# Kernel tuning notes

Measured on AMD Instinct MI355X. Metric: run time of the kernel, lower is better.

## Reference

```python
import jax, jax.numpy as jnp
import numpy as np

B, H, S, D = 1, 16, 8192, 64
WINDOW = 1024  # window_size from init; also used as the query block size


def setup_inputs() -> dict:
    key = jax.random.key(0)
    kq, kk, kv = jax.random.split(key, 3)
    Q = jax.random.normal(kq, (B, H, S, D), dtype=jnp.float32)
    K = jax.random.normal(kk, (B, H, S, D), dtype=jnp.float32)
    V = jax.random.normal(kv, (B, H, S, D), dtype=jnp.float32)
    return {"Q": Q, "K": K, "V": V}


def _sliding_window_attn(Q, K, V, window):
    # Banded causal attention: query q attends kv with 0 <= q - kv <= window.
    # Tile queries into blocks of size W=window; each query block i only needs
    # kv positions [i*W - W, i*W + W), i.e. a 2W-wide local slice. This honors
    # the block-sparse structure instead of materializing an SxS score matrix.
    b, h, s, d = Q.shape
    W = window
    nb = s // W  # number of query blocks
    # Pad K,V by W zeros at the front so every block slice is in-bounds.
    Kp = jnp.pad(K, ((0, 0), (0, 0), (W, 0), (0, 0)))
    Vp = jnp.pad(V, ((0, 0), (0, 0), (W, 0), (0, 0)))
    # Local kv indices for each block: block i covers padded positions [i*W, i*W+2W).
    idx = jnp.arange(nb)[:, None] * W + jnp.arange(2 * W)[None, :]  # [nb, 2W]
    Kb = Kp[:, :, idx, :]  # [B,H,nb,2W,D]
    Vb = Vp[:, :, idx, :]  # [B,H,nb,2W,D]
    Qb = Q.reshape(b, h, nb, W, d)  # [B,H,nb,W,D]

    scale = np.float32(1.0 / np.sqrt(d))  # flex_attention default scaling
    scores = jnp.einsum('bhnqd,bhnkd->bhnqk', Qb, Kb) * scale  # [B,H,nb,W,2W]

    # Global positions: q_global = i*W + qi ; kv_global = i*W + kj - W.
    # Mask conds: q>=kv  <=> qi >= kj - W ;  q-kv<=W  <=> qi <= kj ; kv_global>=0.
    qi = jnp.arange(W)[:, None]          # [W,1]
    kj = jnp.arange(2 * W)[None, :]      # [1,2W]
    rel_mask = (qi <= kj) & (qi >= kj - W)                        # [W,2W]
    kv_global = jnp.arange(nb)[:, None, None] * W + kj[None] - W  # [nb,1,2W]
    mask = rel_mask[None] & (kv_global >= 0)                      # [nb,W,2W]

    neg = jnp.finfo(scores.dtype).min
    scores = jnp.where(mask[None, None], scores, neg)
    attn = jax.nn.softmax(scores, axis=-1)
    out = jnp.einsum('bhnqk,bhnkd->bhnqd', attn, Vb)
    return out.reshape(b, h, s, d)


def reference(Q, K, V):
    return _sliding_window_attn(Q, K, V, WINDOW)
```

## Files before the change

kernel.cpp:

```cpp
#include <hip/hip_runtime.h>
#include <stdint.h>

namespace {
constexpr int kH = 16;
constexpr int kS = 8192;
constexpr int kD = 64;
constexpr int kW = 1024;

typedef __attribute__((ext_vector_type(4)))  float float4_t;
typedef __attribute__((ext_vector_type(16))) float f32x16;
typedef __attribute__((ext_vector_type(8)))  short bf16x8;
typedef __attribute__((ext_vector_type(8)))  short short8_t;

__device__ __forceinline__ unsigned short f2bf(float f) {
    union { float fv; uint32_t u; } c; c.fv = f;
    return (unsigned short)((c.u + 0x7fffu + ((c.u >> 16) & 1u)) >> 16);
}

__device__ __forceinline__ float fexp2(float x) {
#if __has_builtin(__builtin_amdgcn_exp2f)
    return __builtin_amdgcn_exp2f(x);
#else
    return exp2f(x);
#endif
}

__device__ __forceinline__ void gload16(const void* g, char* l) {
    __builtin_amdgcn_global_load_lds(
        (const __attribute__((address_space(1))) void*)g,
        (__attribute__((address_space(3))) void*)l, 16, 0, 0);
}

__global__ __launch_bounds__(256)
void prep_k(const float* __restrict__ K, unsigned short* __restrict__ Kb) {
    const int i = (blockIdx.x * 256 + threadIdx.x) * 8;
    float4_t a = *(const float4_t*)(K + i);
    float4_t b = *(const float4_t*)(K + i + 4);
    short8_t o;
    #pragma unroll
    for (int j = 0; j < 4; ++j) { o[j] = (short)f2bf(a[j]); o[j + 4] = (short)f2bf(b[j]); }
    *(short8_t*)(Kb + i) = o;
}

__global__ __launch_bounds__(256)
void prep_v(const float* __restrict__ V, unsigned short* __restrict__ Vt) {
    __shared__ float tile[64][65];
    const int h = blockIdx.y;
    const int s0 = blockIdx.x * 64;
    const int tid = threadIdx.x;
    const size_t hb = (size_t)h * kS * kD;
    #pragma unroll
    for (int it = 0; it < 4; ++it) {
        const int n = tid + it * 256;
        const int s = n >> 4, d0 = (n & 15) * 4;
        float4_t v = *(const float4_t*)(V + hb + (size_t)(s0 + s) * kD + d0);
        tile[s][d0 + 0] = v[0]; tile[s][d0 + 1] = v[1];
        tile[s][d0 + 2] = v[2]; tile[s][d0 + 3] = v[3];
    }
    __syncthreads();
    #pragma unroll
    for (int it = 0; it < 2; ++it) {
        const int n = tid + it * 256;
        const int d = n >> 3, sc = (n & 7) * 8;
        short8_t o;
        #pragma unroll
        for (int j = 0; j < 8; ++j) o[j] = (short)f2bf(tile[sc + j][d]);
        *(short8_t*)(Vt + (size_t)h * kD * kS + (size_t)d * kS + s0 + sc) = o;
    }
}

__global__ __launch_bounds__(256, 4)
void swa_main(const float* __restrict__ Qg, const unsigned short* __restrict__ Kb,
              const unsigned short* __restrict__ Vt, float* __restrict__ Og) {
    __shared__ __align__(16) char lds[2][16384];

    const int lid  = blockIdx.x;
    const int swz  = (lid & 7) * 128 + (lid >> 3);
    const int h    = swz >> 6;
    const int qblk = swz & 63;

    const int tid  = threadIdx.x;
    const int wv   = tid >> 6;
    const int lane = tid & 63;
    const int lq   = lane & 31;
    const int hi   = lane >> 5;

    const int q0b = qblk * 128;
    const int qs  = q0b + wv * 32;
    const int q   = qs + lq;
    const size_t hb  = (size_t)h * kS * kD;
    const size_t hbv = (size_t)h * kD * kS;

    constexpr float qscale = 0.125f * 1.44269504f;
    bf16x8 qf[4];
    {
        const float* qp = Qg + hb + (size_t)q * kD + hi * 8;
        #pragma unroll
        for (int c = 0; c < 4; ++c) {
            float4_t a = *(const float4_t*)(qp + c * 16);
            float4_t b = *(const float4_t*)(qp + c * 16 + 4);
            bf16x8 f;
            #pragma unroll
            for (int j = 0; j < 4; ++j) {
                f[j]     = (short)f2bf(a[j] * qscale);
                f[j + 4] = (short)f2bf(b[j] * qscale);
            }
            qf[c] = f;
        }
    }

    f32x16 acc[2];
    #pragma unroll
    for (int hf = 0; hf < 2; ++hf)
        #pragma unroll
        for (int r = 0; r < 16; ++r) acc[hf][r] = 0.f;
    float l4[4] = {0.f, 0.f, 0.f, 0.f};

    const int kstart = (q0b >= kW) ? q0b - kW : 0;
    const int nt     = (q0b + 128 - kstart) >> 6;

    int srcK[2], srcV[2];
    #pragma unroll
    for (int i = 0; i < 2; ++i) {
        const int n = tid + i * 256;
        const int c = n ^ ((n >> 3) & 7);
        srcK[i] = (c >> 3) * 64 + (c & 7) * 8;
        srcV[i] = (c >> 3) * kS + (c & 7) * 8;
    }
    const unsigned short* KbH = Kb + hb;
    const unsigned short* VtH = Vt + hbv;

    auto stage = [&](int buf, int kb) {
        const unsigned short* Kt = KbH + (size_t)kb * 64;
        const unsigned short* Vq = VtH + kb;
        #pragma unroll
        for (int i = 0; i < 2; ++i) {
            const int db = i * 4096 + wv * 1024;
            gload16(Kt + srcK[i], &lds[buf][db]);
            gload16(Vq + srcV[i], &lds[buf][8192 + db]);
        }
    };

    stage(0, kstart);
    for (int t = 0; t < nt; ++t) {
        const int kb  = kstart + t * 64;
        const int kbn = (t + 1 < nt) ? kb + 64 : kb;
        stage((t + 1) & 1, kbn);
        asm volatile("s_waitcnt vmcnt(4)" ::: "memory");
        __builtin_amdgcn_s_barrier();
        asm volatile("" ::: "memory");

        const char* Kl = lds[t & 1];
        const char* Vl = lds[t & 1] + 8192;

        #pragma unroll
        for (int half = 0; half < 2; ++half) {
            const int kh = kb + half * 32;
            if (kh <= qs && kh >= qs - kW) {
                const int krow = half * 32 + lq;
                const int ksw  = (krow & 7) << 4;
                bf16x8 kf[4];
                #pragma unroll
                for (int c = 0; c < 4; ++c)
                    kf[c] = *(const bf16x8*)(Kl + ((krow * 128 + c * 32 + hi * 16) ^ ksw));

                f32x16 st;
                #pragma unroll
                for (int r = 0; r < 16; ++r) st[r] = 0.f;
                __builtin_amdgcn_s_setprio(1);
                #pragma unroll
                for (int c = 0; c < 4; ++c)
                    st = __builtin_amdgcn_mfma_f32_32x32x16_bf16(kf[c], qf[c], st, 0, 0, 0);
                __builtin_amdgcn_s_setprio(0);

                const int vsw = (lq & 7) << 4;
                bf16x8 vf[4];
                #pragma unroll
                for (int dh = 0; dh < 2; ++dh)
                    #pragma unroll
                    for (int kc = 0; kc < 2; ++kc)
                        vf[dh * 2 + kc] = *(const bf16x8*)(
                            Vl + (((dh * 32 + lq) * 128 + half * 64 + kc * 32 + hi * 16) ^ vsw));

                float p[16];
                const bool interior = (kh <= qs - 32) && (kh >= qs - 992);
                if (interior) {
                    #pragma unroll
                    for (int r = 0; r < 16; ++r) p[r] = fexp2(st[r]);
                } else {
                    #pragma unroll
                    for (int r = 0; r < 16; ++r) {
                        const int ki = kh + (r & 3) + 8 * (r >> 2) + 4 * hi;
                        const bool ok = (ki <= q) && (ki + kW >= q);
                        const float e = fexp2(st[r]);
                        p[r] = ok ? e : 0.f;
                    }
                }
                #pragma unroll
                for (int r = 0; r < 16; ++r) l4[r & 3] += p[r];

                unsigned int wrd[8];
                #pragma unroll
                for (int j = 0; j < 8; ++j)
                    asm("v_cvt_pk_bf16_f32 %0, %1, %2" : "=v"(wrd[j]) : "v"(p[2 * j]), "v"(p[2 * j + 1]));
                asm("v_permlane32_swap_b32 %0, %1" : "+v"(wrd[0]), "+v"(wrd[2]));
                asm("v_permlane32_swap_b32 %0, %1" : "+v"(wrd[1]), "+v"(wrd[3]));
                asm("v_permlane32_swap_b32 %0, %1" : "+v"(wrd[4]), "+v"(wrd[6]));
                asm("v_permlane32_swap_b32 %0, %1" : "+v"(wrd[5]), "+v"(wrd[7]));
                union U { unsigned int u[4]; bf16x8 v; };
                U u0, u1;
                u0.u[0] = wrd[0]; u0.u[1] = wrd[1]; u0.u[2] = wrd[2]; u0.u[3] = wrd[3];
                u1.u[0] = wrd[4]; u1.u[1] = wrd[5]; u1.u[2] = wrd[6]; u1.u[3] = wrd[7];

                __builtin_amdgcn_s_setprio(1);
                acc[0] = __builtin_amdgcn_mfma_f32_32x32x16_bf16(vf[0], u0.v, acc[0], 0, 0, 0);
                acc[1] = __builtin_amdgcn_mfma_f32_32x32x16_bf16(vf[2], u0.v, acc[1], 0, 0, 0);
                acc[0] = __builtin_amdgcn_mfma_f32_32x32x16_bf16(vf[1], u1.v, acc[0], 0, 0, 0);
                acc[1] = __builtin_amdgcn_mfma_f32_32x32x16_bf16(vf[3], u1.v, acc[1], 0, 0, 0);
                __builtin_amdgcn_s_setprio(0);
            }
        }

        asm volatile("" ::: "memory");
        __builtin_amdgcn_s_barrier();
        asm volatile("" ::: "memory");
    }

    float l = (l4[0] + l4[1]) + (l4[2] + l4[3]);
    l += __shfl_xor(l, 32);
    const float rl = 1.f / l;
    float* op = Og + hb + (size_t)q * kD;
    #pragma unroll
    for (int g = 0; g < 4; ++g) {
        float4_t o0, o1;
        #pragma unroll
        for (int j = 0; j < 4; ++j) {
            o0[j] = acc[0][g * 4 + j] * rl;
            o1[j] = acc[1][g * 4 + j] * rl;
        }
        *(float4_t*)(op + g * 8 + hi * 4)      = o0;
        *(float4_t*)(op + 32 + g * 8 + hi * 4) = o1;
    }
}
}

extern "C" void kernel_launch(void* const* d_in, const int* in_sizes, int n_in,
                              void* d_out, int out_size, void* d_ws, size_t ws_size,
                              hipStream_t stream) {
    (void)in_sizes; (void)n_in; (void)out_size; (void)ws_size;
    const float* Q = (const float*)d_in[0];
    const float* K = (const float*)d_in[1];
    const float* V = (const float*)d_in[2];
    float* O = (float*)d_out;
    unsigned short* Kb = (unsigned short*)d_ws;
    unsigned short* Vt = Kb + (size_t)kH * kS * kD;

    prep_k<<<dim3(kH * kS * kD / 2048), dim3(256), 0, stream>>>(K, Kb);
    prep_v<<<dim3(kS / 64, kH), dim3(256), 0, stream>>>(V, Vt);
    swa_main<<<dim3(1024), dim3(256), 0, stream>>>(Q, Kb, Vt, O);
}
```

Baseline: 71.86 us.

## Fuse K bf16 conversion into attention kernel, dropping separate prep_k pass

```diff
diff --git a/kernel.cpp b/kernel.cpp
--- a/kernel.cpp
+++ b/kernel.cpp
@@ -11,6 +11,7 @@
 typedef __attribute__((ext_vector_type(16))) float f32x16;
 typedef __attribute__((ext_vector_type(8)))  short bf16x8;
 typedef __attribute__((ext_vector_type(8)))  short short8_t;
+typedef __attribute__((ext_vector_type(4)))  unsigned int u32x4;
 
 __device__ __forceinline__ unsigned short f2bf(float f) {
     union { float fv; uint32_t u; } c; c.fv = f;
@@ -31,21 +32,24 @@
         (__attribute__((address_space(3))) void*)l, 16, 0, 0);
 }
 
-__global__ __launch_bounds__(256)
-void prep_k(const float* __restrict__ K, unsigned short* __restrict__ Kb) {
-    const int i = (blockIdx.x * 256 + threadIdx.x) * 8;
-    float4_t a = *(const float4_t*)(K + i);
-    float4_t b = *(const float4_t*)(K + i + 4);
-    short8_t o;
-    #pragma unroll
-    for (int j = 0; j < 4; ++j) { o[j] = (short)f2bf(a[j]); o[j + 4] = (short)f2bf(b[j]); }
-    *(short8_t*)(Kb + i) = o;
-}
+#define P_TO_FRAGS(P, U0, U1)                                                            \
+    {                                                                                    \
+        unsigned int wrd[8];                                                             \
+        _Pragma("unroll")                                                                \
+        for (int j = 0; j < 8; ++j)                                                      \
+            asm("v_cvt_pk_bf16_f32 %0, %1, %2" : "=v"(wrd[j]) : "v"(P[2*j]), "v"(P[2*j+1])); \
+        asm("v_permlane32_swap_b32 %0, %1" : "+v"(wrd[0]), "+v"(wrd[2]));                \
+        asm("v_permlane32_swap_b32 %0, %1" : "+v"(wrd[1]), "+v"(wrd[3]));                \
+        asm("v_permlane32_swap_b32 %0, %1" : "+v"(wrd[4]), "+v"(wrd[6]));                \
+        asm("v_permlane32_swap_b32 %0, %1" : "+v"(wrd[5]), "+v"(wrd[7]));                \
+        U0.u[0] = wrd[0]; U0.u[1] = wrd[1]; U0.u[2] = wrd[2]; U0.u[3] = wrd[3];          \
+        U1.u[0] = wrd[4]; U1.u[1] = wrd[5]; U1.u[2] = wrd[6]; U1.u[3] = wrd[7];          \
+    }
 
 __global__ __launch_bounds__(256)
 void prep_v(const float* __restrict__ V, unsigned short* __restrict__ Vt) {
     __shared__ float tile[64][65];
-    const int h = blockIdx.y;
+    const int h  = blockIdx.y;
     const int s0 = blockIdx.x * 64;
     const int tid = threadIdx.x;
     const size_t hb = (size_t)h * kS * kD;
@@ -65,12 +69,12 @@
         short8_t o;
         #pragma unroll
         for (int j = 0; j < 8; ++j) o[j] = (short)f2bf(tile[sc + j][d]);
-        *(short8_t*)(Vt + (size_t)h * kD * kS + (size_t)d * kS + s0 + sc) = o;
+        *(short8_t*)(Vt + hb + (size_t)d * kS + s0 + sc) = o;
     }
 }
 
 __global__ __launch_bounds__(256, 4)
-void swa_main(const float* __restrict__ Qg, const unsigned short* __restrict__ Kb,
+void swa_main(const float* __restrict__ Qg, const float* __restrict__ Kg,
               const unsigned short* __restrict__ Vt, float* __restrict__ Og) {
     __shared__ __align__(16) char lds[2][16384];
 
@@ -88,8 +92,7 @@
     const int q0b = qblk * 128;
     const int qs  = q0b + wv * 32;
     const int q   = qs + lq;
-    const size_t hb  = (size_t)h * kS * kD;
-    const size_t hbv = (size_t)h * kD * kS;
+    const size_t hb = (size_t)h * kS * kD;
 
     constexpr float qscale = 0.125f * 1.44269504f;
     bf16x8 qf[4];
@@ -111,54 +114,89 @@
 
     f32x16 acc[2];
     #pragma unroll
-    for (int hf = 0; hf < 2; ++hf)
-        #pragma unroll
-        for (int r = 0; r < 16; ++r) acc[hf][r] = 0.f;
+    for (int r = 0; r < 16; ++r) { acc[0][r] = 0.f; acc[1][r] = 0.f; }
     float l4[4] = {0.f, 0.f, 0.f, 0.f};
 
     const int kstart = (q0b >= kW) ? q0b - kW : 0;
     const int nt     = (q0b + 128 - kstart) >> 6;
 
-    int srcK[2], srcV[2];
+    const int r0 = tid >> 3, g8 = (tid & 7) * 8;
+    const int r1 = r0 + 32;
+    const int kdst0 = (r0 * 128 + g8 * 2) ^ ((r0 & 7) << 4);
+    const int kdst1 = (r1 * 128 + g8 * 2) ^ ((r1 & 7) << 4);
+    const float* KgH = Kg + hb;
+
+    int srcV[2];
     #pragma unroll
     for (int i = 0; i < 2; ++i) {
         const int n = tid + i * 256;
         const int c = n ^ ((n >> 3) & 7);
-        srcK[i] = (c >> 3) * 64 + (c & 7) * 8;
         srcV[i] = (c >> 3) * kS + (c & 7) * 8;
     }
-    const unsigned short* KbH = Kb + hb;
-    const unsigned short* VtH = Vt + hbv;
-
-    auto stage = [&](int buf, int kb) {
-        const unsigned short* Kt = KbH + (size_t)kb * 64;
-        const unsigned short* Vq = VtH + kb;
-        #pragma unroll
-        for (int i = 0; i < 2; ++i) {
-            const int db = i * 4096 + wv * 1024;
-            gload16(Kt + srcK[i], &lds[buf][db]);
-            gload16(Vq + srcV[i], &lds[buf][8192 + db]);
-        }
-    };
-
-    stage(0, kstart);
+    const unsigned short* VtH = Vt + hb;
+
+    float4_t k0lo, k0hi, k1lo, k1hi;
+
+    union U { unsigned int u[4]; bf16x8 v; };
+
+#define LOAD_K(KB)                                                         \
+    {                                                                      \
+        const float* p0_ = KgH + (size_t)((KB) + r0) * kD + g8;            \
+        const float* p1_ = KgH + (size_t)((KB) + r1) * kD + g8;            \
+        k0lo = *(const float4_t*)(p0_);                                    \
+        k0hi = *(const float4_t*)(p0_ + 4);                                \
+        k1lo = *(const float4_t*)(p1_);                                    \
+        k1hi = *(const float4_t*)(p1_ + 4);                                \
+    }
+
+#define STAGE_V(BUF, KB)                                                   \
+    {                                                                      \
+        const unsigned short* vq_ = VtH + (KB);                            \
+        gload16(vq_ + srcV[0], &lds[BUF][8192 + wv * 1024]);               \
+        gload16(vq_ + srcV[1], &lds[BUF][8192 + 4096 + wv * 1024]);        \
+    }
+
+#define CVT_WRITE_K(BUF)                                                   \
+    {                                                                      \
+        unsigned int w0_, w1_, w2_, w3_;                                   \
+        u32x4 wv0_, wv1_;                                                  \
+        asm("v_cvt_pk_bf16_f32 %0, %1, %2" : "=v"(w0_) : "v"(k0lo[0]), "v"(k0lo[1])); \
+        asm("v_cvt_pk_bf16_f32 %0, %1, %2" : "=v"(w1_) : "v"(k0lo[2]), "v"(k0lo[3])); \
+        asm("v_cvt_pk_bf16_f32 %0, %1, %2" : "=v"(w2_) : "v"(k0hi[0]), "v"(k0hi[1])); \
+        asm("v_cvt_pk_bf16_f32 %0, %1, %2" : "=v"(w3_) : "v"(k0hi[2]), "v"(k0hi[3])); \
+        wv0_[0] = w0_; wv0_[1] = w1_; wv0_[2] = w2_; wv0_[3] = w3_;        \
+        asm("v_cvt_pk_bf16_f32 %0, %1, %2" : "=v"(w0_) : "v"(k1lo[0]), "v"(k1lo[1])); \
+        asm("v_cvt_pk_bf16_f32 %0, %1, %2" : "=v"(w1_) : "v"(k1lo[2]), "v"(k1lo[3])); \
+        asm("v_cvt_pk_bf16_f32 %0, %1, %2" : "=v"(w2_) : "v"(k1hi[0]), "v"(k1hi[1])); \
+        asm("v_cvt_pk_bf16_f32 %0, %1, %2" : "=v"(w3_) : "v"(k1hi[2]), "v"(k1hi[3])); \
+        wv1_[0] = w0_; wv1_[1] = w1_; wv1_[2] = w2_; wv1_[3] = w3_;        \
+        *(u32x4*)(&lds[BUF][kdst0]) = wv0_;                                \
+        *(u32x4*)(&lds[BUF][kdst1]) = wv1_;                                \
+    }
+
+    LOAD_K(kstart);
+    STAGE_V(0, kstart);
+    asm volatile("s_waitcnt vmcnt(2)" ::: "memory");
+    CVT_WRITE_K(0);
+
     for (int t = 0; t < nt; ++t) {
         const int kb  = kstart + t * 64;
         const int kbn = (t + 1 < nt) ? kb + 64 : kb;
-        stage((t + 1) & 1, kbn);
-        asm volatile("s_waitcnt vmcnt(4)" ::: "memory");
+        LOAD_K(kbn);
+        STAGE_V((t + 1) & 1, kbn);
+        asm volatile("s_waitcnt vmcnt(6) lgkmcnt(0)" ::: "memory");
         __builtin_amdgcn_s_barrier();
         asm volatile("" ::: "memory");
 
         const char* Kl = lds[t & 1];
         const char* Vl = lds[t & 1] + 8192;
+        const int ksw = (lq & 7) << 4;
 
         #pragma unroll
         for (int half = 0; half < 2; ++half) {
             const int kh = kb + half * 32;
             if (kh <= qs && kh >= qs - kW) {
                 const int krow = half * 32 + lq;
-                const int ksw  = (krow & 7) << 4;
                 bf16x8 kf[4];
                 #pragma unroll
                 for (int c = 0; c < 4; ++c)
@@ -173,14 +211,13 @@
                     st = __builtin_amdgcn_mfma_f32_32x32x16_bf16(kf[c], qf[c], st, 0, 0, 0);
                 __builtin_amdgcn_s_setprio(0);
 
-                const int vsw = (lq & 7) << 4;
                 bf16x8 vf[4];
                 #pragma unroll
                 for (int dh = 0; dh < 2; ++dh)
                     #pragma unroll
                     for (int kc = 0; kc < 2; ++kc)
                         vf[dh * 2 + kc] = *(const bf16x8*)(
-                            Vl + (((dh * 32 + lq) * 128 + half * 64 + kc * 32 + hi * 16) ^ vsw));
+                            Vl + (((dh * 32 + lq) * 128 + half * 64 + kc * 32 + hi * 16) ^ ksw));
 
                 float p[16];
                 const bool interior = (kh <= qs - 32) && (kh >= qs - 992);
@@ -199,18 +236,8 @@
                 #pragma unroll
                 for (int r = 0; r < 16; ++r) l4[r & 3] += p[r];
 
-                unsigned int wrd[8];
-                #pragma unroll
-                for (int j = 0; j < 8; ++j)
-                    asm("v_cvt_pk_bf16_f32 %0, %1, %2" : "=v"(wrd[j]) : "v"(p[2 * j]), "v"(p[2 * j + 1]));
-                asm("v_permlane32_swap_b32 %0, %1" : "+v"(wrd[0]), "+v"(wrd[2]));
-                asm("v_permlane32_swap_b32 %0, %1" : "+v"(wrd[1]), "+v"(wrd[3]));
-                asm("v_permlane32_swap_b32 %0, %1" : "+v"(wrd[4]), "+v"(wrd[6]));
-                asm("v_permlane32_swap_b32 %0, %1" : "+v"(wrd[5]), "+v"(wrd[7]));
-                union U { unsigned int u[4]; bf16x8 v; };
                 U u0, u1;
-                u0.u[0] = wrd[0]; u0.u[1] = wrd[1]; u0.u[2] = wrd[2]; u0.u[3] = wrd[3];
-                u1.u[0] = wrd[4]; u1.u[1] = wrd[5]; u1.u[2] = wrd[6]; u1.u[3] = wrd[7];
+                P_TO_FRAGS(p, u0, u1);
 
                 __builtin_amdgcn_s_setprio(1);
                 acc[0] = __builtin_amdgcn_mfma_f32_32x32x16_bf16(vf[0], u0.v, acc[0], 0, 0, 0);
@@ -221,6 +248,9 @@
             }
         }
 
+        asm volatile("s_waitcnt vmcnt(2)" ::: "memory");
+        CVT_WRITE_K((t + 1) & 1);
+
         asm volatile("" ::: "memory");
         __builtin_amdgcn_s_barrier();
         asm volatile("" ::: "memory");
@@ -241,6 +271,9 @@
         *(float4_t*)(op + g * 8 + hi * 4)      = o0;
         *(float4_t*)(op + 32 + g * 8 + hi * 4) = o1;
     }
+#undef LOAD_K
+#undef STAGE_V
+#undef CVT_WRITE_K
 }
 }
 
@@ -252,10 +285,8 @@
     const float* K = (const float*)d_in[1];
     const float* V = (const float*)d_in[2];
     float* O = (float*)d_out;
-    unsigned short* Kb = (unsigned short*)d_ws;
-    unsigned short* Vt = Kb + (size_t)kH * kS * kD;
-
-    prep_k<<<dim3(kH * kS * kD / 2048), dim3(256), 0, stream>>>(K, Kb);
+    unsigned short* Vt = (unsigned short*)d_ws;
+
     prep_v<<<dim3(kS / 64, kH), dim3(256), 0, stream>>>(V, Vt);
-    swa_main<<<dim3(1024), dim3(256), 0, stream>>>(Q, Kb, Vt, O);
-}
+    swa_main<<<dim3(1024), dim3(256), 0, stream>>>(Q, K, Vt, O);
+}
```

Result: slower. 79.37 us (+10.5%).
